# Kernel tuning notes

Measured on AMD Instinct MI355X. Metric: run time of the kernel, lower is better.

The kernel has to match this reference:

```python
import jax, jax.numpy as jnp
import numpy as np
from jax.scipy.special import erf

ALPHA = 0.84
SSIM_WIN = 11       # monai SSIMLoss default win_size
SIGMA = 1.5         # both kernels use sigma=1.5
K1, K2, DATA_RANGE = 0.01, 0.03, 1.0


def _erf_gauss_1d(sigma=SIGMA, truncated=4.0):
    # monai.networks.layers.gaussian_1d, approx='erf', normalize=False
    tail = int(max(sigma * truncated, 0.5) + 0.5)  # 6 -> 13 taps
    x = jnp.arange(-tail, tail + 1, dtype=jnp.float32)
    t = 0.70710678 / sigma
    out = 0.5 * (erf(t * (x + 0.5)) - erf(t * (x - 0.5)))
    return jnp.clip(out, 0.0)


def _ssim_gauss_1d(win=SSIM_WIN, sigma=SIGMA):
    # monai SSIM gaussian kernel: exp-based, normalized
    d = jnp.arange(-(win - 1) / 2.0, (win + 1) / 2.0, dtype=jnp.float32)
    g = jnp.exp(-(d ** 2) / (2.0 * sigma ** 2))
    return g / g.sum()


def _conv1d(x, k, axis, pad):
    # depthwise 1D conv along spatial axis of NCHW tensor (C=1)
    ks = k.shape[0]
    if axis == 2:
        kern = k.reshape(1, 1, ks, 1)
        p = [(pad, pad), (0, 0)]
    else:
        kern = k.reshape(1, 1, 1, ks)
        p = [(0, 0), (pad, pad)]
    return jax.lax.conv_general_dilated(
        x, kern, window_strides=(1, 1), padding=p,
        dimension_numbers=('NCHW', 'OIHW', 'NCHW'))


def _sep_filter(x, k, pad):
    return _conv1d(_conv1d(x, k, 2, pad), k, 3, pad)


def setup_inputs() -> dict:
    key = jax.random.key(0)
    kx, ky = jax.random.split(key)
    shape = (64, 1, 512, 512)
    x = jax.random.uniform(kx, shape, dtype=jnp.float32)
    y = jax.random.uniform(ky, shape, dtype=jnp.float32)
    return {"x": x, "y": y}


def reference(x, y):
    kw = _ssim_gauss_1d()
    filt = lambda t: _sep_filter(t, kw, 0)
    c1 = (K1 * DATA_RANGE) ** 2
    c2 = (K2 * DATA_RANGE) ** 2
    mx, my = filt(x), filt(y)
    mxx, myy, mxy = filt(x * x), filt(y * y), filt(x * y)
    vx = mxx - mx * mx
    vy = myy - my * my
    cov = mxy - mx * my
    ssim = ((2.0 * mx * my + c1) * (2.0 * cov + c2)) / (
        (mx * mx + my * my + c1) * (vx + vy + c2))
    ssim_loss = 1.0 - jnp.mean(ssim)  # scalar, reduction='mean'

    # --- L1 branch: SAME zero-padded erf-gaussian filtering, no reduction ---
    ke = _erf_gauss_1d()
    pad = (ke.shape[0] - 1) // 2
    l1 = jnp.abs(_sep_filter(y, ke, pad) - _sep_filter(x, ke, pad))  # [N,1,H,W]

    return 100.0 * (ALPHA * ssim_loss + (1.0 - ALPHA) * l1)
```

## Files before the change

kernel.cpp:

```cpp
#include <hip/hip_runtime.h>
#include <cmath>

#define IMG_W 512
#define IMG_H 512
#define NIMG 64
#define OWV 502

struct KTaps {
    float kw[11];
    float ke[13];
};

__global__ __launch_bounds__(256) void ssim_band_kernel(
        const float* __restrict__ x, const float* __restrict__ y,
        double* __restrict__ ssum, KTaps kt) {
    __shared__ __align__(16) float sx[2][272];
    __shared__ __align__(16) float sy[2][272];

    const int img   = blockIdx.z;
    const int band  = blockIdx.y;
    const int strip = blockIdx.x;
    const int tid   = threadIdx.x;
    const int r0    = band * 64;
    const int c0    = strip * 256;

    const float* __restrict__ xi = x + (size_t)img * IMG_H * IMG_W;
    const float* __restrict__ yi = y + (size_t)img * IMG_H * IMG_W;

    float w12[12];
#pragma unroll
    for (int j = 0; j < 12; ++j) w12[j] = 0.f;
    if (tid & 1) {
#pragma unroll
        for (int j = 0; j < 11; ++j) w12[j + 1] = kt.kw[j];
    } else {
#pragma unroll
        for (int j = 0; j < 11; ++j) w12[j] = kt.kw[j];
    }

    float acc[11][5];
#pragma unroll
    for (int i = 0; i < 11; ++i)
#pragma unroll
        for (int q = 0; q < 5; ++q) acc[i][q] = 0.f;
    float tsum = 0.f;

    const int basei = tid & ~1;
    const int outc  = c0 + tid;

    auto ldx = [&](int r, int g) -> float2 {
        float2 v = make_float2(0.f, 0.f);
        if (r < IMG_H && g < IMG_W) v = *(const float2*)(xi + (size_t)r * IMG_W + g);
        return v;
    };
    auto ldy = [&](int r, int g) -> float2 {
        float2 v = make_float2(0.f, 0.f);
        if (r < IMG_H && g < IMG_W) v = *(const float2*)(yi + (size_t)r * IMG_W + g);
        return v;
    };

    if (tid < 133) { float2 v = ldx(r0, c0 + 2 * tid); *(float2*)&sx[0][2 * tid] = v; }
    if (tid >= 123) { const int t3 = tid - 123; float2 v = ldy(r0, c0 + 2 * t3); *(float2*)&sy[0][2 * t3] = v; }
    __syncthreads();

#pragma unroll 1
    for (int chunk = 0; chunk < 7; ++chunk) {
#pragma unroll
        for (int p = 0; p < 11; ++p) {
            const int rr = chunk * 11 + p;
            if (rr <= 73) {
                const int b = rr & 1;
                float2 px = make_float2(0.f, 0.f), py = make_float2(0.f, 0.f);
                const bool pre = (rr < 73);
                if (pre) {
                    if (tid < 133) px = ldx(r0 + rr + 1, c0 + 2 * tid);
                    if (tid >= 123) py = ldy(r0 + rr + 1, c0 + 2 * (tid - 123));
                }
                float xv[12], yv[12];
#pragma unroll
                for (int j = 0; j < 6; ++j) {
                    const float2 a = *(const float2*)&sx[b][basei + 2 * j];
                    const float2 c = *(const float2*)&sy[b][basei + 2 * j];
                    xv[2 * j] = a.x; xv[2 * j + 1] = a.y;
                    yv[2 * j] = c.x; yv[2 * j + 1] = c.y;
                }
                float h0 = 0.f, h1 = 0.f, h2 = 0.f, h3 = 0.f, h4 = 0.f;
#pragma unroll
                for (int j = 0; j < 12; ++j) {
                    const float w = w12[j];
                    const float a = xv[j], bb = yv[j];
                    h0 += w * a;
                    h1 += w * bb;
                    h2 += w * (a * a);
                    h3 += w * (bb * bb);
                    h4 += w * (a * bb);
                }
#pragma unroll
                for (int d = 0; d <= 10; ++d) {
                    const int s = (p + 11 - d) % 11;
                    const float w = kt.kw[d];
                    acc[s][0] += w * h0; acc[s][1] += w * h1; acc[s][2] += w * h2;
                    acc[s][3] += w * h3; acc[s][4] += w * h4;
                }
                {
                    const int sc = (p + 1) % 11;
                    const int ro = rr - 10;
                    if (ro >= 0) {
                        const int o = r0 + ro;
                        if (o < OWV && outc < OWV) {
                            const float mx = acc[sc][0], my = acc[sc][1];
                            const float vx = acc[sc][2] - mx * mx;
                            const float vy = acc[sc][3] - my * my;
                            const float cov = acc[sc][4] - mx * my;
                            const float c1 = 1e-4f, c2 = 9e-4f;
                            tsum += ((2.f * mx * my + c1) * (2.f * cov + c2)) /
                                    ((mx * mx + my * my + c1) * (vx + vy + c2));
                        }
                    }
#pragma unroll
                    for (int q = 0; q < 5; ++q) acc[sc][q] = 0.f;
                }
                if (pre) {
                    const int bn = b ^ 1;
                    if (tid < 133) *(float2*)&sx[bn][2 * tid] = px;
                    if (tid >= 123) *(float2*)&sy[bn][2 * (tid - 123)] = py;
                }
                __syncthreads();
            }
        }
    }

#pragma unroll
    for (int off = 32; off > 0; off >>= 1) tsum += __shfl_down(tsum, off, 64);
    __shared__ float wsum[4];
    const int wid = tid >> 6, lane = tid & 63;
    if (lane == 0) wsum[wid] = tsum;
    __syncthreads();
    if (tid == 0) atomicAdd(ssum, (double)(wsum[0] + wsum[1] + wsum[2] + wsum[3]));
}

__global__ __launch_bounds__(256) void l1_band_kernel(
        const float* __restrict__ x, const float* __restrict__ y,
        const double* __restrict__ ssum, float* __restrict__ out, KTaps kt) {
    __shared__ __align__(16) float sd[2][528];

    const int img  = blockIdx.y;
    const int band = blockIdx.x;
    const int tid  = threadIdx.x;
    const int o0   = band * 32;
    const int rin0 = o0 - 6;

    const float* __restrict__ xi = x + (size_t)img * IMG_H * IMG_W;
    const float* __restrict__ yi = y + (size_t)img * IMG_H * IMG_W;
    float* __restrict__ oi = out + (size_t)img * IMG_H * IMG_W;

    const float base = 100.f * 0.84f * (1.f - (float)(*ssum) * (1.f / 16128256.f));

    float acc[13][2];
#pragma unroll
    for (int i = 0; i < 13; ++i) { acc[i][0] = 0.f; acc[i][1] = 0.f; }

    if (tid < 12) {
        const int idx = (tid < 6) ? tid : (512 + tid);
        sd[0][idx] = 0.f; sd[1][idx] = 0.f;
    }

    auto ldd = [&](int r) -> float2 {
        float2 v = make_float2(0.f, 0.f);
        if (r >= 0 && r < IMG_H) {
            const float2 a = *(const float2*)(xi + (size_t)r * IMG_W + 2 * tid);
            const float2 bb = *(const float2*)(yi + (size_t)r * IMG_W + 2 * tid);
            v = make_float2(bb.x - a.x, bb.y - a.y);
        }
        return v;
    };

    { float2 v = ldd(rin0); *(float2*)&sd[0][6 + 2 * tid] = v; }
    __syncthreads();

#pragma unroll 1
    for (int chunk = 0; chunk < 4; ++chunk) {
#pragma unroll
        for (int p = 0; p < 13; ++p) {
            const int rr = chunk * 13 + p;
            if (rr <= 43) {
                const int b = rr & 1;
                float2 pv = make_float2(0.f, 0.f);
                const bool pre = (rr < 43);
                if (pre) pv = ldd(rin0 + rr + 1);

                float dv[14];
#pragma unroll
                for (int j = 0; j < 7; ++j) {
                    const float2 a = *(const float2*)&sd[b][2 * tid + 2 * j];
                    dv[2 * j] = a.x; dv[2 * j + 1] = a.y;
                }
                float a0 = 0.f, a1 = 0.f;
#pragma unroll
                for (int u = 0; u < 13; ++u) {
                    a0 += kt.ke[u] * dv[u];
                    a1 += kt.ke[u] * dv[u + 1];
                }
#pragma unroll
                for (int dd = 0; dd <= 12; ++dd) {
                    const int s = (p + 13 - dd) % 13;
                    acc[s][0] += kt.ke[dd] * a0;
                    acc[s][1] += kt.ke[dd] * a1;
                }
                {
                    const int sc = (p + 1) % 13;
                    const int ro = rr - 12;
                    if (ro >= 0) {
                        const int o = o0 + ro;
                        *(float2*)&oi[(size_t)o * IMG_W + 2 * tid] =
                            make_float2(base + 16.f * fabsf(acc[sc][0]),
                                        base + 16.f * fabsf(acc[sc][1]));
                    }
                    acc[sc][0] = 0.f; acc[sc][1] = 0.f;
                }
                if (pre) *(float2*)&sd[b ^ 1][6 + 2 * tid] = pv;
                __syncthreads();
            }
        }
    }
}

extern "C" void kernel_launch(void* const* d_in, const int* in_sizes, int n_in,
                              void* d_out, int out_size, void* d_ws, size_t ws_size,
                              hipStream_t stream) {
    const float* x = (const float*)d_in[0];
    const float* y = (const float*)d_in[1];
    float* out = (float*)d_out;
    double* ssum = (double*)d_ws;

    KTaps kt;
    {
        double g[11], s = 0.0;
        for (int i = 0; i < 11; ++i) {
            const double d = (double)i - 5.0;
            g[i] = std::exp(-(d * d) / 4.5);
            s += g[i];
        }
        for (int i = 0; i < 11; ++i) kt.kw[i] = (float)(g[i] / s);
    }
    {
        const double t = 0.70710678 / 1.5;
        for (int i = 0; i < 13; ++i) {
            const double xx = (double)i - 6.0;
            const double v = 0.5 * (std::erf(t * (xx + 0.5)) - std::erf(t * (xx - 0.5)));
            kt.ke[i] = (float)(v < 0.0 ? 0.0 : v);
        }
    }

    hipMemsetAsync(ssum, 0, sizeof(double), stream);

    ssim_band_kernel<<<dim3(2, 8, NIMG), dim3(256), 0, stream>>>(x, y, ssum, kt);
    l1_band_kernel<<<dim3(16, NIMG, 1), dim3(256), 0, stream>>>(x, y, ssum, out, kt);
}
```

Measured before the change: 301.8 us.

## Give each wave private LDS row buffers and replace block barriers with wave fences

Both band kernels now split the shared row buffer into per-wave slices, each holding that wave's columns plus its own halo. This lets the per-row __syncthreads be replaced by a wave-level barrier, so the four waves in a block no longer stall on each other. The global prefetch is moved one row further ahead and written into the alternate buffer right after the current row is read. The cost is duplicated halo loads across waves and reliance on wave-synchronous LDS ordering for correctness.

```diff
diff --git a/kernel.cpp b/kernel.cpp
--- a/kernel.cpp
+++ b/kernel.cpp
@@ -11,26 +11,48 @@
     float ke[13];
 };
 
+#define WAVE_FENCE() __builtin_amdgcn_wave_barrier()
+
 __global__ __launch_bounds__(256) void ssim_band_kernel(
         const float* __restrict__ x, const float* __restrict__ y,
         double* __restrict__ ssum, KTaps kt) {
-    __shared__ __align__(16) float sx[2][272];
-    __shared__ __align__(16) float sy[2][272];
+    __shared__ __align__(16) float sxw[4][2][80];
+    __shared__ __align__(16) float syw[4][2][80];
 
     const int img   = blockIdx.z;
     const int band  = blockIdx.y;
     const int strip = blockIdx.x;
     const int tid   = threadIdx.x;
+    const int w     = tid >> 6;
+    const int lane  = tid & 63;
     const int r0    = band * 64;
-    const int c0    = strip * 256;
+    const int wc0   = strip * 256 + w * 64;
 
     const float* __restrict__ xi = x + (size_t)img * IMG_H * IMG_W;
     const float* __restrict__ yi = y + (size_t)img * IMG_H * IMG_W;
 
+    const bool xon  = (lane < 38);
+    const bool yon  = (lane >= 26);
+    const int  xcol = wc0 + 2 * lane;
+    const int  ycol = wc0 + 2 * (lane - 26);
+    const bool xok  = xon && (xcol < IMG_W);
+    const bool yok  = yon && (ycol < IMG_W);
+
+    auto ldx2 = [&](int r) -> float2 {
+        float2 v = make_float2(0.f, 0.f);
+        if (xok && r < IMG_H) v = *(const float2*)(xi + (size_t)r * IMG_W + xcol);
+        return v;
+    };
+    auto ldy2 = [&](int r) -> float2 {
+        float2 v = make_float2(0.f, 0.f);
+        if (yok && r < IMG_H) v = *(const float2*)(yi + (size_t)r * IMG_W + ycol);
+        return v;
+    };
+
     float w12[12];
 #pragma unroll
     for (int j = 0; j < 12; ++j) w12[j] = 0.f;
-    if (tid & 1) {
+    if (lane & 1) {
 #pragma unroll
         for (int j = 0; j < 11; ++j) w12[j + 1] = kt.kw[j];
     } else {
@@ -45,23 +67,18 @@
         for (int q = 0; q < 5; ++q) acc[i][q] = 0.f;
     float tsum = 0.f;
 
-    const int basei = tid & ~1;
-    const int outc  = c0 + tid;
-
-    auto ldx = [&](int r, int g) -> float2 {
-        float2 v = make_float2(0.f, 0.f);
-        if (r < IMG_H && g < IMG_W) v = *(const float2*)(xi + (size_t)r * IMG_W + g);
-        return v;
-    };
-    auto ldy = [&](int r, int g) -> float2 {
-        float2 v = make_float2(0.f, 0.f);
-        if (r < IMG_H && g < IMG_W) v = *(const float2*)(yi + (size_t)r * IMG_W + g);
-        return v;
-    };
-
-    if (tid < 133) { float2 v = ldx(r0, c0 + 2 * tid); *(float2*)&sx[0][2 * tid] = v; }
-    if (tid >= 123) { const int t3 = tid - 123; float2 v = ldy(r0, c0 + 2 * t3); *(float2*)&sy[0][2 * t3] = v; }
-    __syncthreads();
+    const int basei = lane & ~1;
+    const int outc  = wc0 + lane;
+
+    {
+        const float2 vx = ldx2(r0);
+        const float2 vy = ldy2(r0);
+        if (xon) *(float2*)&sxw[w][0][2 * lane] = vx;
+        if (yon) *(float2*)&syw[w][0][2 * (lane - 26)] = vy;
+    }
+    float2 pfx = ldx2(r0 + 1);
+    float2 pfy = ldy2(r0 + 1);
+    WAVE_FENCE();
 
 #pragma unroll 1
     for (int chunk = 0; chunk < 7; ++chunk) {
@@ -70,37 +87,39 @@
             const int rr = chunk * 11 + p;
             if (rr <= 73) {
                 const int b = rr & 1;
-                float2 px = make_float2(0.f, 0.f), py = make_float2(0.f, 0.f);
-                const bool pre = (rr < 73);
-                if (pre) {
-                    if (tid < 133) px = ldx(r0 + rr + 1, c0 + 2 * tid);
-                    if (tid >= 123) py = ldy(r0 + rr + 1, c0 + 2 * (tid - 123));
-                }
                 float xv[12], yv[12];
 #pragma unroll
                 for (int j = 0; j < 6; ++j) {
-                    const float2 a = *(const float2*)&sx[b][basei + 2 * j];
-                    const float2 c = *(const float2*)&sy[b][basei + 2 * j];
+                    const float2 a = *(const float2*)&sxw[w][b][basei + 2 * j];
+                    const float2 c = *(const float2*)&syw[w][b][basei + 2 * j];
                     xv[2 * j] = a.x; xv[2 * j + 1] = a.y;
                     yv[2 * j] = c.x; yv[2 * j + 1] = c.y;
                 }
+                if (rr < 73) {
+                    if (xon) *(float2*)&sxw[w][b ^ 1][2 * lane] = pfx;
+                    if (yon) *(float2*)&syw[w][b ^ 1][2 * (lane - 26)] = pfy;
+                }
+                if (rr < 72) {
+                    pfx = ldx2(r0 + rr + 2);
+                    pfy = ldy2(r0 + rr + 2);
+                }
                 float h0 = 0.f, h1 = 0.f, h2 = 0.f, h3 = 0.f, h4 = 0.f;
 #pragma unroll
                 for (int j = 0; j < 12; ++j) {
-                    const float w = w12[j];
+                    const float wj = w12[j];
                     const float a = xv[j], bb = yv[j];
-                    h0 += w * a;
-                    h1 += w * bb;
-                    h2 += w * (a * a);
-                    h3 += w * (bb * bb);
-                    h4 += w * (a * bb);
+                    h0 += wj * a;
+                    h1 += wj * bb;
+                    h2 += wj * (a * a);
+                    h3 += wj * (bb * bb);
+                    h4 += wj * (a * bb);
                 }
 #pragma unroll
                 for (int d = 0; d <= 10; ++d) {
                     const int s = (p + 11 - d) % 11;
-                    const float w = kt.kw[d];
-                    acc[s][0] += w * h0; acc[s][1] += w * h1; acc[s][2] += w * h2;
-                    acc[s][3] += w * h3; acc[s][4] += w * h4;
+                    const float wv = kt.kw[d];
+                    acc[s][0] += wv * h0; acc[s][1] += wv * h1; acc[s][2] += wv * h2;
+                    acc[s][3] += wv * h3; acc[s][4] += wv * h4;
                 }
                 {
                     const int sc = (p + 1) % 11;
@@ -120,12 +139,7 @@
 #pragma unroll
                     for (int q = 0; q < 5; ++q) acc[sc][q] = 0.f;
                 }
-                if (pre) {
-                    const int bn = b ^ 1;
-                    if (tid < 133) *(float2*)&sx[bn][2 * tid] = px;
-                    if (tid >= 123) *(float2*)&sy[bn][2 * (tid - 123)] = py;
-                }
-                __syncthreads();
+                WAVE_FENCE();
             }
         }
     }
@@ -133,8 +147,7 @@
 #pragma unroll
     for (int off = 32; off > 0; off >>= 1) tsum += __shfl_down(tsum, off, 64);
     __shared__ float wsum[4];
-    const int wid = tid >> 6, lane = tid & 63;
-    if (lane == 0) wsum[wid] = tsum;
+    if (lane == 0) wsum[w] = tsum;
     __syncthreads();
     if (tid == 0) atomicAdd(ssum, (double)(wsum[0] + wsum[1] + wsum[2] + wsum[3]));
 }
@@ -142,13 +155,16 @@
 __global__ __launch_bounds__(256) void l1_band_kernel(
         const float* __restrict__ x, const float* __restrict__ y,
         const double* __restrict__ ssum, float* __restrict__ out, KTaps kt) {
-    __shared__ __align__(16) float sd[2][528];
+    __shared__ __align__(16) float sdw[4][2][144];
 
     const int img  = blockIdx.y;
     const int band = blockIdx.x;
     const int tid  = threadIdx.x;
+    const int w    = tid >> 6;
+    const int lane = tid & 63;
     const int o0   = band * 32;
     const int rin0 = o0 - 6;
+    const int wc0  = w * 128;
 
     const float* __restrict__ xi = x + (size_t)img * IMG_H * IMG_W;
     const float* __restrict__ yi = y + (size_t)img * IMG_H * IMG_W;
@@ -156,27 +172,36 @@
 
     const float base = 100.f * 0.84f * (1.f - (float)(*ssum) * (1.f / 16128256.f));
 
-    float acc[13][2];
-#pragma unroll
-    for (int i = 0; i < 13; ++i) { acc[i][0] = 0.f; acc[i][1] = 0.f; }
-
-    if (tid < 12) {
-        const int idx = (tid < 6) ? tid : (512 + tid);
-        sd[0][idx] = 0.f; sd[1][idx] = 0.f;
-    }
-
-    auto ldd = [&](int r) -> float2 {
+    const int  g0  = wc0 - 6 + 2 * lane;
+    const bool ok0 = (g0 >= 0) && (g0 < IMG_W);
+    const bool on1 = (lane >= 58);
+    const int  g1  = wc0 + 6 + 2 * lane;
+    const bool ok1 = on1 && (g1 < IMG_W);
+    const int  i1  = 128 + 2 * (lane - 58);
+
+    auto ldd = [&](int r, bool ok, int g) -> float2 {
         float2 v = make_float2(0.f, 0.f);
-        if (r >= 0 && r < IMG_H) {
-            const float2 a = *(const float2*)(xi + (size_t)r * IMG_W + 2 * tid);
-            const float2 bb = *(const float2*)(yi + (size_t)r * IMG_W + 2 * tid);
+        if (ok && r >= 0 && r < IMG_H) {
+            const float2 a  = *(const float2*)(xi + (size_t)r * IMG_W + g);
+            const float2 bb = *(const float2*)(yi + (size_t)r * IMG_W + g);
             v = make_float2(bb.x - a.x, bb.y - a.y);
         }
         return v;
     };
 
-    { float2 v = ldd(rin0); *(float2*)&sd[0][6 + 2 * tid] = v; }
-    __syncthreads();
+    float acc[13][2];
+#pragma unroll
+    for (int i = 0; i < 13; ++i) { acc[i][0] = 0.f; acc[i][1] = 0.f; }
+
+    {
+        const float2 v0 = ldd(rin0, ok0, g0);
+        const float2 v1 = ldd(rin0, ok1, g1);
+        *(float2*)&sdw[w][0][2 * lane] = v0;
+        if (on1) *(float2*)&sdw[w][0][i1] = v1;
+    }
+    float2 pf0 = ldd(rin0 + 1, ok0, g0);
+    float2 pf1 = ldd(rin0 + 1, ok1, g1);
+    WAVE_FENCE();
 
 #pragma unroll 1
     for (int chunk = 0; chunk < 4; ++chunk) {
@@ -185,15 +210,19 @@
             const int rr = chunk * 13 + p;
             if (rr <= 43) {
                 const int b = rr & 1;
-                float2 pv = make_float2(0.f, 0.f);
-                const bool pre = (rr < 43);
-                if (pre) pv = ldd(rin0 + rr + 1);
-
                 float dv[14];
 #pragma unroll
                 for (int j = 0; j < 7; ++j) {
-                    const float2 a = *(const float2*)&sd[b][2 * tid + 2 * j];
+                    const float2 a = *(const float2*)&sdw[w][b][2 * lane + 2 * j];
                     dv[2 * j] = a.x; dv[2 * j + 1] = a.y;
+                }
+                if (rr < 43) {
+                    *(float2*)&sdw[w][b ^ 1][2 * lane] = pf0;
+                    if (on1) *(float2*)&sdw[w][b ^ 1][i1] = pf1;
+                }
+                if (rr < 42) {
+                    pf0 = ldd(rin0 + rr + 2, ok0, g0);
+                    pf1 = ldd(rin0 + rr + 2, ok1, g1);
                 }
                 float a0 = 0.f, a1 = 0.f;
 #pragma unroll
@@ -212,14 +241,13 @@
                     const int ro = rr - 12;
                     if (ro >= 0) {
                         const int o = o0 + ro;
-                        *(float2*)&oi[(size_t)o * IMG_W + 2 * tid] =
+                        *(float2*)&oi[(size_t)o * IMG_W + wc0 + 2 * lane] =
                             make_float2(base + 16.f * fabsf(acc[sc][0]),
                                         base + 16.f * fabsf(acc[sc][1]));
                     }
                     acc[sc][0] = 0.f; acc[sc][1] = 0.f;
                 }
-                if (pre) *(float2*)&sd[b ^ 1][6 + 2 * tid] = pv;
-                __syncthreads();
+                WAVE_FENCE();
             }
         }
     }
```

Result: faster. 287.3 us (-4.8%).

## Use per-wave private LDS tiles with wave barriers instead of block syncs

Applied to the files above, without the earlier changes.

Both kernels now give each 64-lane wave its own LDS tile with a halo, so per-row staging needs only a wave-level fence instead of a block-wide __syncthreads. The SSIM kernel also folds the xx/yy/xy statistics into (x+y)^2 and (x-y)^2, cutting the filtered quantities from five to four. It uses a hardware reciprocal and prefetches two rows ahead. The L1 kernel switches to one output column per lane and doubles the grid by splitting columns into strips. The costs are redundant halo loads per wave, reduced precision from the squared-sum reformulation and the approximate reciprocal, and a reliance on wave-synchronous LDS ordering being correct.

```diff
diff --git a/kernel.cpp b/kernel.cpp
--- a/kernel.cpp
+++ b/kernel.cpp
@@ -11,121 +11,112 @@
     float ke[13];
 };
 
+#define WAVE_FENCE() __builtin_amdgcn_wave_barrier()
+
 __global__ __launch_bounds__(256) void ssim_band_kernel(
         const float* __restrict__ x, const float* __restrict__ y,
         double* __restrict__ ssum, KTaps kt) {
-    __shared__ __align__(16) float sx[2][272];
-    __shared__ __align__(16) float sy[2][272];
+    __shared__ __align__(16) float sq[4][2][4][80];
 
     const int img   = blockIdx.z;
     const int band  = blockIdx.y;
     const int strip = blockIdx.x;
     const int tid   = threadIdx.x;
+    const int w     = tid >> 6;
+    const int lane  = tid & 63;
     const int r0    = band * 64;
-    const int c0    = strip * 256;
+    const int wc0   = strip * 256 + w * 64;
 
     const float* __restrict__ xi = x + (size_t)img * IMG_H * IMG_W;
     const float* __restrict__ yi = y + (size_t)img * IMG_H * IMG_W;
 
-    float w12[12];
-#pragma unroll
-    for (int j = 0; j < 12; ++j) w12[j] = 0.f;
-    if (tid & 1) {
-#pragma unroll
-        for (int j = 0; j < 11; ++j) w12[j + 1] = kt.kw[j];
-    } else {
-#pragma unroll
-        for (int j = 0; j < 11; ++j) w12[j] = kt.kw[j];
-    }
-
-    float acc[11][5];
+    const bool stg = (lane < 38);
+    const int  gc  = wc0 + 2 * lane;
+    const bool gok = stg && (gc < IMG_W);
+
+    auto ld2 = [&](const float* __restrict__ p, int r) -> float2 {
+        float2 v = make_float2(0.f, 0.f);
+        if (gok && r < IMG_H) v = *(const float2*)(p + (size_t)r * IMG_W + gc);
+        return v;
+    };
+
+    auto stage = [&](int buf, float2 vx, float2 vy) {
+        if (stg) {
+            const float s0 = vx.x + vy.x, d0 = vx.x - vy.x;
+            const float s1 = vx.y + vy.y, d1 = vx.y - vy.y;
+            *(float2*)&sq[w][buf][0][2 * lane] = vx;
+            *(float2*)&sq[w][buf][1][2 * lane] = vy;
+            *(float2*)&sq[w][buf][2][2 * lane] = make_float2(s0 * s0, s1 * s1);
+            *(float2*)&sq[w][buf][3][2 * lane] = make_float2(d0 * d0, d1 * d1);
+        }
+    };
+
+    float acc[11][4];
 #pragma unroll
     for (int i = 0; i < 11; ++i)
 #pragma unroll
-        for (int q = 0; q < 5; ++q) acc[i][q] = 0.f;
+        for (int q = 0; q < 4; ++q) acc[i][q] = 0.f;
     float tsum = 0.f;
-
-    const int basei = tid & ~1;
-    const int outc  = c0 + tid;
-
-    auto ldx = [&](int r, int g) -> float2 {
-        float2 v = make_float2(0.f, 0.f);
-        if (r < IMG_H && g < IMG_W) v = *(const float2*)(xi + (size_t)r * IMG_W + g);
-        return v;
-    };
-    auto ldy = [&](int r, int g) -> float2 {
-        float2 v = make_float2(0.f, 0.f);
-        if (r < IMG_H && g < IMG_W) v = *(const float2*)(yi + (size_t)r * IMG_W + g);
-        return v;
-    };
-
-    if (tid < 133) { float2 v = ldx(r0, c0 + 2 * tid); *(float2*)&sx[0][2 * tid] = v; }
-    if (tid >= 123) { const int t3 = tid - 123; float2 v = ldy(r0, c0 + 2 * t3); *(float2*)&sy[0][2 * t3] = v; }
-    __syncthreads();
+    const int outc = wc0 + lane;
+
+    stage(0, ld2(xi, r0), ld2(yi, r0));
+    float2 pfx[2], pfy[2];
+    pfx[1] = ld2(xi, r0 + 1); pfy[1] = ld2(yi, r0 + 1);
+    pfx[0] = ld2(xi, r0 + 2); pfy[0] = ld2(yi, r0 + 2);
+    WAVE_FENCE();
 
 #pragma unroll 1
-    for (int chunk = 0; chunk < 7; ++chunk) {
-#pragma unroll
-        for (int p = 0; p < 11; ++p) {
-            const int rr = chunk * 11 + p;
+    for (int c2 = 0; c2 < 4; ++c2) {
+        const int rbase = c2 * 22;
+#pragma unroll
+        for (int p22 = 0; p22 < 22; ++p22) {
+            const int rr  = rbase + p22;
+            const int p11 = p22 % 11;
+            const int b   = p22 & 1;
             if (rr <= 73) {
-                const int b = rr & 1;
-                float2 px = make_float2(0.f, 0.f), py = make_float2(0.f, 0.f);
-                const bool pre = (rr < 73);
-                if (pre) {
-                    if (tid < 133) px = ldx(r0 + rr + 1, c0 + 2 * tid);
-                    if (tid >= 123) py = ldy(r0 + rr + 1, c0 + 2 * (tid - 123));
-                }
-                float xv[12], yv[12];
-#pragma unroll
-                for (int j = 0; j < 6; ++j) {
-                    const float2 a = *(const float2*)&sx[b][basei + 2 * j];
-                    const float2 c = *(const float2*)&sy[b][basei + 2 * j];
-                    xv[2 * j] = a.x; xv[2 * j + 1] = a.y;
-                    yv[2 * j] = c.x; yv[2 * j + 1] = c.y;
-                }
-                float h0 = 0.f, h1 = 0.f, h2 = 0.f, h3 = 0.f, h4 = 0.f;
-#pragma unroll
-                for (int j = 0; j < 12; ++j) {
-                    const float w = w12[j];
-                    const float a = xv[j], bb = yv[j];
-                    h0 += w * a;
-                    h1 += w * bb;
-                    h2 += w * (a * a);
-                    h3 += w * (bb * bb);
-                    h4 += w * (a * bb);
+                float h[4];
+#pragma unroll
+                for (int q = 0; q < 4; ++q) {
+                    float a0 = 0.f;
+#pragma unroll
+                    for (int u = 0; u < 11; ++u)
+                        a0 += kt.kw[u] * sq[w][b][q][lane + u];
+                    h[q] = a0;
+                }
+                if (rr < 73) stage(b ^ 1, pfx[(p22 + 1) & 1], pfy[(p22 + 1) & 1]);
+                if (rr < 71) {
+                    pfx[(p22 + 1) & 1] = ld2(xi, r0 + rr + 3);
+                    pfy[(p22 + 1) & 1] = ld2(yi, r0 + rr + 3);
                 }
 #pragma unroll
                 for (int d = 0; d <= 10; ++d) {
-                    const int s = (p + 11 - d) % 11;
-                    const float w = kt.kw[d];
-                    acc[s][0] += w * h0; acc[s][1] += w * h1; acc[s][2] += w * h2;
-                    acc[s][3] += w * h3; acc[s][4] += w * h4;
+                    const int s = (p11 + 11 - d) % 11;
+                    const float wv = kt.kw[d];
+                    acc[s][0] += wv * h[0]; acc[s][1] += wv * h[1];
+                    acc[s][2] += wv * h[2]; acc[s][3] += wv * h[3];
                 }
                 {
-                    const int sc = (p + 1) % 11;
+                    const int sc = (p11 + 1) % 11;
                     const int ro = rr - 10;
                     if (ro >= 0) {
                         const int o = r0 + ro;
                         if (o < OWV && outc < OWV) {
                             const float mx = acc[sc][0], my = acc[sc][1];
-                            const float vx = acc[sc][2] - mx * mx;
-                            const float vy = acc[sc][3] - my * my;
-                            const float cov = acc[sc][4] - mx * my;
-                            const float c1 = 1e-4f, c2 = 9e-4f;
-                            tsum += ((2.f * mx * my + c1) * (2.f * cov + c2)) /
-                                    ((mx * mx + my * my + c1) * (vx + vy + c2));
+                            const float Aq = acc[sc][2], Bq = acc[sc][3];
+                            const float mq   = mx * mx + my * my;
+                            const float pxy  = mx * my;
+                            const float vsum = 0.5f  * (Aq + Bq) - mq;
+                            const float cov  = 0.25f * (Aq - Bq) - pxy;
+                            const float c1 = 1e-4f, c2c = 9e-4f;
+                            const float num = (2.f * pxy + c1) * (2.f * cov + c2c);
+                            const float den = (mq + c1) * (vsum + c2c);
+                            tsum += num * __builtin_amdgcn_rcpf(den);
                         }
                     }
 #pragma unroll
-                    for (int q = 0; q < 5; ++q) acc[sc][q] = 0.f;
-                }
-                if (pre) {
-                    const int bn = b ^ 1;
-                    if (tid < 133) *(float2*)&sx[bn][2 * tid] = px;
-                    if (tid >= 123) *(float2*)&sy[bn][2 * (tid - 123)] = py;
-                }
-                __syncthreads();
+                    for (int q = 0; q < 4; ++q) acc[sc][q] = 0.f;
+                }
+                WAVE_FENCE();
             }
         }
     }
@@ -133,22 +124,26 @@
 #pragma unroll
     for (int off = 32; off > 0; off >>= 1) tsum += __shfl_down(tsum, off, 64);
     __shared__ float wsum[4];
-    const int wid = tid >> 6, lane = tid & 63;
-    if (lane == 0) wsum[wid] = tsum;
+    if (lane == 0) wsum[w] = tsum;
     __syncthreads();
     if (tid == 0) atomicAdd(ssum, (double)(wsum[0] + wsum[1] + wsum[2] + wsum[3]));
 }
 
-__global__ __launch_bounds__(256) void l1_band_kernel(
+__global__ __launch_bounds__(256, 8) void l1_band_kernel(
         const float* __restrict__ x, const float* __restrict__ y,
         const double* __restrict__ ssum, float* __restrict__ out, KTaps kt) {
-    __shared__ __align__(16) float sd[2][528];
-
-    const int img  = blockIdx.y;
-    const int band = blockIdx.x;
-    const int tid  = threadIdx.x;
-    const int o0   = band * 32;
-    const int rin0 = o0 - 6;
+    __shared__ __align__(16) float sdw[4][2][80];
+
+    const int img   = blockIdx.y;
+    const int bx    = blockIdx.x;
+    const int strip = bx & 1;
+    const int band  = bx >> 1;
+    const int tid   = threadIdx.x;
+    const int w     = tid >> 6;
+    const int lane  = tid & 63;
+    const int o0    = band * 32;
+    const int rin0  = o0 - 6;
+    const int wc0   = strip * 256 + w * 64;
 
     const float* __restrict__ xi = x + (size_t)img * IMG_H * IMG_W;
     const float* __restrict__ yi = y + (size_t)img * IMG_H * IMG_W;
@@ -156,70 +151,62 @@
 
     const float base = 100.f * 0.84f * (1.f - (float)(*ssum) * (1.f / 16128256.f));
 
-    float acc[13][2];
-#pragma unroll
-    for (int i = 0; i < 13; ++i) { acc[i][0] = 0.f; acc[i][1] = 0.f; }
-
-    if (tid < 12) {
-        const int idx = (tid < 6) ? tid : (512 + tid);
-        sd[0][idx] = 0.f; sd[1][idx] = 0.f;
-    }
-
-    auto ldd = [&](int r) -> float2 {
+    const bool stg = (lane < 38);
+    const int  gc  = wc0 - 6 + 2 * lane;
+    const bool gok = stg && (gc >= 0) && (gc < IMG_W);
+
+    auto ld2 = [&](const float* __restrict__ p, int r) -> float2 {
         float2 v = make_float2(0.f, 0.f);
-        if (r >= 0 && r < IMG_H) {
-            const float2 a = *(const float2*)(xi + (size_t)r * IMG_W + 2 * tid);
-            const float2 bb = *(const float2*)(yi + (size_t)r * IMG_W + 2 * tid);
-            v = make_float2(bb.x - a.x, bb.y - a.y);
-        }
+        if (gok && r >= 0 && r < IMG_H) v = *(const float2*)(p + (size_t)r * IMG_W + gc);
         return v;
     };
-
-    { float2 v = ldd(rin0); *(float2*)&sd[0][6 + 2 * tid] = v; }
-    __syncthreads();
+    auto stage = [&](int buf, float2 vx, float2 vy) {
+        if (stg) *(float2*)&sdw[w][buf][2 * lane] =
+            make_float2(vy.x - vx.x, vy.y - vx.y);
+    };
+
+    float acc[13];
+#pragma unroll
+    for (int i = 0; i < 13; ++i) acc[i] = 0.f;
+
+    stage(0, ld2(xi, rin0), ld2(yi, rin0));
+    float2 pfx[2], pfy[2];
+    pfx[1] = ld2(xi, rin0 + 1); pfy[1] = ld2(yi, rin0 + 1);
+    pfx[0] = ld2(xi, rin0 + 2); pfy[0] = ld2(yi, rin0 + 2);
+    WAVE_FENCE();
 
 #pragma unroll 1
-    for (int chunk = 0; chunk < 4; ++chunk) {
-#pragma unroll
-        for (int p = 0; p < 13; ++p) {
-            const int rr = chunk * 13 + p;
+    for (int c2 = 0; c2 < 2; ++c2) {
+        const int rbase = c2 * 26;
+#pragma unroll
+        for (int p26 = 0; p26 < 26; ++p26) {
+            const int rr  = rbase + p26;
+            const int p13 = p26 % 13;
+            const int b   = p26 & 1;
             if (rr <= 43) {
-                const int b = rr & 1;
-                float2 pv = make_float2(0.f, 0.f);
-                const bool pre = (rr < 43);
-                if (pre) pv = ldd(rin0 + rr + 1);
-
-                float dv[14];
-#pragma unroll
-                for (int j = 0; j < 7; ++j) {
-                    const float2 a = *(const float2*)&sd[b][2 * tid + 2 * j];
-                    dv[2 * j] = a.x; dv[2 * j + 1] = a.y;
-                }
-                float a0 = 0.f, a1 = 0.f;
-#pragma unroll
-                for (int u = 0; u < 13; ++u) {
-                    a0 += kt.ke[u] * dv[u];
-                    a1 += kt.ke[u] * dv[u + 1];
-                }
-#pragma unroll
-                for (int dd = 0; dd <= 12; ++dd) {
-                    const int s = (p + 13 - dd) % 13;
-                    acc[s][0] += kt.ke[dd] * a0;
-                    acc[s][1] += kt.ke[dd] * a1;
-                }
+                float a0 = 0.f;
+#pragma unroll
+                for (int u = 0; u < 13; ++u)
+                    a0 += kt.ke[u] * sdw[w][b][lane + u];
+                if (rr < 43) stage(b ^ 1, pfx[(p26 + 1) & 1], pfy[(p26 + 1) & 1]);
+                if (rr < 41) {
+                    pfx[(p26 + 1) & 1] = ld2(xi, rin0 + rr + 3);
+                    pfy[(p26 + 1) & 1] = ld2(yi, rin0 + rr + 3);
+                }
+#pragma unroll
+                for (int d = 0; d <= 12; ++d)
+                    acc[(p13 + 13 - d) % 13] += kt.ke[d] * a0;
                 {
-                    const int sc = (p + 1) % 13;
+                    const int sc = (p13 + 1) % 13;
                     const int ro = rr - 12;
                     if (ro >= 0) {
                         const int o = o0 + ro;
-                        *(float2*)&oi[(size_t)o * IMG_W + 2 * tid] =
-                            make_float2(base + 16.f * fabsf(acc[sc][0]),
-                                        base + 16.f * fabsf(acc[sc][1]));
+                        oi[(size_t)o * IMG_W + wc0 + lane] =
+                            fmaf(16.f, fabsf(acc[sc]), base);
                     }
-                    acc[sc][0] = 0.f; acc[sc][1] = 0.f;
-                }
-                if (pre) *(float2*)&sd[b ^ 1][6 + 2 * tid] = pv;
-                __syncthreads();
+                    acc[sc] = 0.f;
+                }
+                WAVE_FENCE();
             }
         }
     }
@@ -255,5 +242,5 @@
     hipMemsetAsync(ssum, 0, sizeof(double), stream);
 
     ssim_band_kernel<<<dim3(2, 8, NIMG), dim3(256), 0, stream>>>(x, y, ssum, kt);
-    l1_band_kernel<<<dim3(16, NIMG, 1), dim3(256), 0, stream>>>(x, y, ssum, out, kt);
+    l1_band_kernel<<<dim3(32, NIMG, 1), dim3(256), 0, stream>>>(x, y, ssum, out, kt);
 }
```

After: 288.0 us. -4.6%, faster.
